# Performance work log

Hardware: AMD Instinct MI355X
Metric: run time of the kernel (lower is better)

## Reference

```python
import jax, jax.numpy as jnp
import numpy as np

LMAX = 3
D_IRREP = (LMAX + 1) ** 2  # 16
EPS = 1e-5


def _conv1d(x, w, pad):
    # x: [N, C_in, L], w: [C_out, C_in, K] -> [N, C_out, L]
    return jax.lax.conv_general_dilated(
        x, w, window_strides=(1,), padding=[(pad, pad)],
        dimension_numbers=("NCH", "OIH", "NCH"))


def setup_inputs() -> dict:
    key = jax.random.key(0)
    ks = jax.random.split(key, 8)
    B, Cin, Cout, N, K, RES = 128, 256, 256, 64, 5, 8
    return {
        "x": jax.random.normal(ks[0], (B, Cin * D_IRREP, N), jnp.float32),
        "weight": jax.random.normal(ks[1], (LMAX + 1, Cout, Cin, K), jnp.float32) / np.sqrt(Cin * K).astype(np.float32),
        "bias": jax.random.normal(ks[2], (1, 1, Cout), jnp.float32) * 0.02,
        "affine_weight": jnp.ones((LMAX + 1, Cout), jnp.float32),
        "gating_w": jax.random.normal(ks[3], (Cout, Cout), jnp.float32) / np.sqrt(Cout).astype(np.float32),
        "gating_b": jnp.zeros((Cout,), jnp.float32),
        "to_grid": jax.random.normal(ks[4], (RES, RES, D_IRREP), jnp.float32) * 0.3,
        "from_grid": jax.random.normal(ks[5], (RES, RES, D_IRREP), jnp.float32) * 0.3,
    }


def reference(x, weight, bias, affine_weight, gating_w, gating_b, to_grid, from_grid):
    B, CI, N = x.shape
    Cin = CI // D_IRREP
    Cout = weight.shape[1]
    pad = weight.shape[-1] // 2
    x = x.reshape(B, Cin, D_IRREP, N)

    # per-degree Conv1d over the time axis, irrep order folded into batch
    h_parts = []
    for l in range(LMAX + 1):
        lo, li = l * l, 2 * l + 1
        x_l = x[:, :, lo:lo + li, :]                                  # [B, Cin, li, N]
        x_l = x_l.transpose(0, 2, 1, 3).reshape(B * li, Cin, N)       # (b i) c n
        h_l = _conv1d(x_l, weight[l], pad)                            # [B*li, Cout, N]
        h_l = h_l.reshape(B, li, Cout, N).transpose(0, 3, 1, 2).reshape(B * N, li, Cout)  # (b n) i c
        if l == 0:
            h_l = h_l + bias
        h_parts.append(h_l)
    h = jnp.concatenate(h_parts, axis=1)                              # [B*N, 16, Cout]

    # rms_norm_sh: center l=0 over channels, degree-balanced RMS, per-degree affine
    degrees = np.repeat(np.arange(LMAX + 1), 2 * np.arange(LMAX + 1) + 1)  # [16]
    bal = jnp.asarray((1.0 / (2.0 * degrees + 1.0)) / (LMAX + 1), h.dtype)  # [16]
    mean0 = jnp.mean(h[:, :1, :], axis=2, keepdims=True)
    h = jnp.concatenate([h[:, :1, :] - mean0, h[:, 1:, :]], axis=1)
    var = jnp.einsum("zic,i->zc", h * h, bal)                         # [Z, C]
    inv = jax.lax.rsqrt(jnp.mean(var, axis=-1)[:, None, None] + EPS)  # [Z,1,1]
    h = h * inv * affine_weight[degrees][None]                        # [Z,16,C]

    # SeparableS2Activation: SiLU-gated scalars + S2 grid activation for l>0
    gate = jax.nn.silu(h[:, :1, :] @ gating_w.T + gating_b)           # [Z,1,C]
    grid = jax.nn.silu(jnp.einsum("bai,zic->zbac", to_grid, h))       # [Z,8,8,C]
    s2 = jnp.einsum("bai,zbac->zic", from_grid, grid)                 # [Z,16,C]
    h = jnp.concatenate([gate, s2[:, 1:, :]], axis=1)

    # (b n) i c -> b (c i) n
    out = h.reshape(B, N, D_IRREP, Cout).transpose(0, 3, 2, 1).reshape(B, Cout * D_IRREP, N)
    return out
```

## Files before the change

### kernel.cpp

```cpp
#include <hip/hip_runtime.h>
#include <hip/hip_bf16.h>

#define BB    128
#define CIN   256
#define COUT  256
#define NN    64
#define KW    5
#define DIRR  16
#define ZTOT  (BB*NN)
#define SX    264

typedef __attribute__((ext_vector_type(4))) float f32x4;
typedef __attribute__((ext_vector_type(8))) short s16x8;

__device__ inline ushort f2bf(float f) {
    __hip_bfloat16 h = __float2bfloat16(f);
    return *(const ushort*)&h;
}
__device__ inline float bf2f(ushort u) {
    union { unsigned int ui; float f; } cv; cv.ui = ((unsigned int)u) << 16;
    return cv.f;
}
__device__ inline float wave_sum(float v) {
    #pragma unroll
    for (int o = 32; o > 0; o >>= 1) v += __shfl_down(v, o, 64);
    return v;
}
__device__ inline float silu(float x) { return x / (1.f + __expf(-x)); }

__global__ __launch_bounds__(256) void pack_w_k(const float* __restrict__ w,
                                                ushort* __restrict__ wb)
{
    int idx = blockIdx.x * 256 + threadIdx.x;
    int cl = idx & 31;
    int c  = (idx >> 5) & 255;
    int ch = (idx >> 13) & 7;
    int k  = (idx >> 16) % 5;
    int l  = idx / 327680;
    int cin = ch * 32 + cl;
    wb[idx] = f2bf(w[(((size_t)(l * COUT + c) * CIN) + cin) * KW + k]);
}

__global__ __launch_bounds__(256) void pack2_k(const float* __restrict__ gw,
                                               const float* __restrict__ tg,
                                               const float* __restrict__ fg,
                                               ushort* __restrict__ gwb,
                                               ushort* __restrict__ tgb,
                                               ushort* __restrict__ fgTb)
{
    int idx = blockIdx.x * 256 + threadIdx.x;
    if (idx < 65536) {
        gwb[idx] = f2bf(gw[idx]);
    } else if (idx < 66560) {
        int j = idx - 65536;
        tgb[j] = f2bf(tg[j]);
    } else if (idx < 67584) {
        int j = idx - 66560;
        int p = j >> 4, i = j & 15;
        fgTb[i * 64 + p] = f2bf(fg[j]);
    }
}

__global__ __launch_bounds__(256, 4) void conv_mfma_k(const float* __restrict__ x,
                                                      const ushort* __restrict__ wb,
                                                      const float* __restrict__ bias,
                                                      ushort* __restrict__ hbuf)
{
    __shared__ __align__(16) ushort xs[68 * SX];

    const int tid  = threadIdx.x;
    const int lane = tid & 63;
    const int wid  = tid >> 6;
    const int blk  = blockIdx.x;
    const int b = blk >> 4, i = blk & 15;
    const int l = (i == 0) ? 0 : (i < 4) ? 1 : (i < 9) ? 2 : 3;

    {
        const float4* xb = (const float4*)(x + (((size_t)b * CIN) * DIRR + i) * NN);
        #pragma unroll
        for (int p = 0; p < 16; ++p) {
            int cin = (tid & 63) | ((p & 3) << 6);
            int nq  = ((tid >> 6) << 2) | (p >> 2);
            float4 v = xb[(size_t)cin * (DIRR * NN / 4) + nq];
            ushort* dst = xs + (size_t)(2 + nq * 4) * SX + cin;
            dst[0]      = f2bf(v.x);
            dst[SX]     = f2bf(v.y);
            dst[2 * SX] = f2bf(v.z);
            dst[3 * SX] = f2bf(v.w);
        }
        xs[ 0 * SX + tid] = 0; xs[ 1 * SX + tid] = 0;
        xs[66 * SX + tid] = 0; xs[67 * SX + tid] = 0;
    }
    __syncthreads();

    f32x4 acc[4][4];
    #pragma unroll
    for (int m = 0; m < 4; ++m)
        #pragma unroll
        for (int j = 0; j < 4; ++j) acc[m][j] = (f32x4){0.f, 0.f, 0.f, 0.f};

    const int kb = lane >> 4;
    const int lr = lane & 15;

    const ushort* wl = wb + (size_t)l * (40 * 8192);
    int boffB[4];
    #pragma unroll
    for (int j = 0; j < 4; ++j)
        boffB[j] = (wid * 64 + j * 16 + lr) * 32 + kb * 8;

    const ushort* arow = xs + (size_t)lr * SX + kb * 8;

    s16x8 bva[4], bvb[4];
    {
        const ushort* bt = wl;
        #pragma unroll
        for (int j = 0; j < 4; ++j) bva[j] = *(const s16x8*)(bt + boffB[j]);
    }

    #pragma unroll 1
    for (int t = 0; t < 40; t += 2) {
        {
            const ushort* bt = wl + ((size_t)(t + 1) << 13);
            #pragma unroll
            for (int j = 0; j < 4; ++j) bvb[j] = *(const s16x8*)(bt + boffB[j]);
        }
        {
            const ushort* ab = arow + (size_t)(t >> 3) * SX + (t & 7) * 32;
            s16x8 av[4];
            #pragma unroll
            for (int m = 0; m < 4; ++m)
                av[m] = *(const s16x8*)(ab + (size_t)m * 16 * SX);
            #pragma unroll
            for (int m = 0; m < 4; ++m)
                #pragma unroll
                for (int j = 0; j < 4; ++j)
                    acc[m][j] = __builtin_amdgcn_mfma_f32_16x16x32_bf16(av[m], bva[j], acc[m][j], 0, 0, 0);
        }
        if (t + 2 < 40) {
            const ushort* bt = wl + ((size_t)(t + 2) << 13);
            #pragma unroll
            for (int j = 0; j < 4; ++j) bva[j] = *(const s16x8*)(bt + boffB[j]);
        }
        {
            int t1 = t + 1;
            const ushort* ab = arow + (size_t)(t1 >> 3) * SX + (t1 & 7) * 32;
            s16x8 av[4];
            #pragma unroll
            for (int m = 0; m < 4; ++m)
                av[m] = *(const s16x8*)(ab + (size_t)m * 16 * SX);
            #pragma unroll
            for (int m = 0; m < 4; ++m)
                #pragma unroll
                for (int j = 0; j < 4; ++j)
                    acc[m][j] = __builtin_amdgcn_mfma_f32_16x16x32_bf16(av[m], bvb[j], acc[m][j], 0, 0, 0);
        }
    }

    const int row0 = (lane >> 4) * 4;
    #pragma unroll
    for (int j = 0; j < 4; ++j) {
        int c = wid * 64 + j * 16 + lr;
        float bvv = (i == 0) ? bias[c] : 0.f;
        #pragma unroll
        for (int m = 0; m < 4; ++m)
            #pragma unroll
            for (int r = 0; r < 4; ++r) {
                int n = m * 16 + row0 + r;
                size_t z = (size_t)b * NN + n;
                hbuf[(z * DIRR + i) * COUT + c] = f2bf(acc[m][j][r] + bvv);
            }
    }
}

__global__ __launch_bounds__(256) void norm_k(const ushort* __restrict__ hbuf,
                                              const float* __restrict__ afw,
                                              ushort* __restrict__ hn2,
                                              ushort* __restrict__ hn0)
{
    __shared__ float red[8];
    const int z0 = blockIdx.x * 2;
    const int c = threadIdx.x;
    const int lane = c & 63, w = c >> 6;

    float hv[2][16];
    #pragma unroll
    for (int zz = 0; zz < 2; ++zz)
        #pragma unroll
        for (int i = 0; i < 16; ++i)
            hv[zz][i] = bf2f(hbuf[((size_t)(z0 + zz) * DIRR + i) * COUT + c]);

    float s0 = wave_sum(hv[0][0]);
    float s1 = wave_sum(hv[1][0]);
    if (lane == 0) { red[w] = s0; red[4 + w] = s1; }
    __syncthreads();
    float m0 = (red[0] + red[1] + red[2] + red[3]) * (1.f / 256.f);
    float m1 = (red[4] + red[5] + red[6] + red[7]) * (1.f / 256.f);
    hv[0][0] -= m0;
    hv[1][0] -= m1;

    const float bal[4] = {0.25f, 1.f / 12.f, 1.f / 20.f, 1.f / 28.f};
    float var[2];
    #pragma unroll
    for (int zz = 0; zz < 2; ++zz) {
        float v = bal[0] * hv[zz][0] * hv[zz][0];
        #pragma unroll
        for (int i = 1; i < 16; ++i) {
            int li = (i < 4) ? 1 : (i < 9) ? 2 : 3;
            v += bal[li] * hv[zz][i] * hv[zz][i];
        }
        var[zz] = v;
    }
    float v0 = wave_sum(var[0]);
    float v1 = wave_sum(var[1]);
    __syncthreads();
    if (lane == 0) { red[w] = v0; red[4 + w] = v1; }
    __syncthreads();
    float inv[2];
    inv[0] = rsqrtf((red[0] + red[1] + red[2] + red[3]) * (1.f / 256.f) + 1e-5f);
    inv[1] = rsqrtf((red[4] + red[5] + red[6] + red[7]) * (1.f / 256.f) + 1e-5f);

    float a0 = afw[c], a1 = afw[COUT + c], a2 = afw[2 * COUT + c], a3 = afw[3 * COUT + c];
    #pragma unroll
    for (int zz = 0; zz < 2; ++zz) {
        s16x8 o0, o1;
        #pragma unroll
        for (int i = 0; i < 16; ++i) {
            float al = (i == 0) ? a0 : (i < 4) ? a1 : (i < 9) ? a2 : a3;
            ushort ub = f2bf(hv[zz][i] * inv[zz] * al);
            if (i < 8) o0[i] = (short)ub; else o1[i - 8] = (short)ub;
        }
        ushort* dst = hn2 + ((size_t)c * ZTOT + z0 + zz) * DIRR;
        *(s16x8*)dst = o0;
        *(s16x8*)(dst + 8) = o1;
        hn0[(size_t)(z0 + zz) * COUT + c] = (ushort)(unsigned short)o0[0];
    }
}

__global__ __launch_bounds__(256) void gate_k(const ushort* __restrict__ hn0,
                                              const ushort* __restrict__ gwb,
                                              const float* __restrict__ gb,
                                              float* __restrict__ out)
{
    const int b = blockIdx.x;
    const int tid = threadIdx.x;
    const int lane = tid & 63, w = tid >> 6;
    const int lr = lane & 15, kb = lane >> 4;

    f32x4 acc[4][4];
    #pragma unroll
    for (int m = 0; m < 4; ++m)
        #pragma unroll
        for (int n = 0; n < 4; ++n) acc[m][n] = (f32x4){0.f, 0.f, 0.f, 0.f};

    #pragma unroll 1
    for (int ks = 0; ks < 8; ++ks) {
        s16x8 av[4], bv[4];
        #pragma unroll
        for (int m = 0; m < 4; ++m)
            av[m] = *(const s16x8*)(hn0 + ((size_t)(b * 64 + m * 16 + lr) * 256 + ks * 32 + kb * 8));
        #pragma unroll
        for (int n = 0; n < 4; ++n)
            bv[n] = *(const s16x8*)(gwb + ((size_t)(w * 64 + n * 16 + lr) * 256 + ks * 32 + kb * 8));
        #pragma unroll
        for (int m = 0; m < 4; ++m)
            #pragma unroll
            for (int n = 0; n < 4; ++n)
                acc[m][n] = __builtin_amdgcn_mfma_f32_16x16x32_bf16(av[m], bv[n], acc[m][n], 0, 0, 0);
    }

    #pragma unroll
    for (int n = 0; n < 4; ++n) {
        int c = w * 64 + n * 16 + lr;
        float gbc = gb[c];
        #pragma unroll
        for (int m = 0; m < 4; ++m)
            #pragma unroll
            for (int r = 0; r < 4; ++r) {
                int nrow = m * 16 + kb * 4 + r;
                out[((size_t)b * COUT + c) * (DIRR * NN) + nrow] = silu(acc[m][n][r] + gbc);
            }
    }
}

__global__ __launch_bounds__(256) void grid_k(const ushort* __restrict__ hn2,
                                              const ushort* __restrict__ tgb,
                                              const ushort* __restrict__ fgTb,
                                              float* __restrict__ out)
{
    __shared__ __align__(16) char lds[36864 + 2048 + 2304];
    ushort* P_s  = (ushort*)lds;
    float*  S_s  = (float*)lds;
    ushort* tg_s = (ushort*)(lds + 36864);
    ushort* fgT_s= (ushort*)(lds + 36864 + 2048);

    const int bid = blockIdx.x;
    const int c  = bid & 255;
    const int zt = bid >> 8;
    const int z0 = zt * 256;
    const int tid = threadIdx.x;
    const int lane = tid & 63, w = tid >> 6;
    const int lr = lane & 15, kb = lane >> 4;

    #pragma unroll
    for (int q = 0; q < 4; ++q) {
        int idx = q * 256 + tid;
        tg_s[idx] = tgb[idx];
        int i = idx >> 6, p = idx & 63;
        fgT_s[i * 72 + p] = fgTb[idx];
    }
    __syncthreads();

    f32x4 acc[4][4];
    #pragma unroll
    for (int m = 0; m < 4; ++m)
        #pragma unroll
        for (int n = 0; n < 4; ++n) acc[m][n] = (f32x4){0.f, 0.f, 0.f, 0.f};

    s16x8 bv[4];
    #pragma unroll
    for (int n = 0; n < 4; ++n)
        bv[n] = (kb < 2) ? *(const s16x8*)(tg_s + (n * 16 + lr) * 16 + kb * 8)
                         : (s16x8){0,0,0,0,0,0,0,0};
    #pragma unroll
    for (int m = 0; m < 4; ++m) {
        int zl = w * 64 + m * 16 + lr;
        s16x8 av = (kb < 2) ? *(const s16x8*)(hn2 + ((size_t)c * ZTOT + z0 + zl) * DIRR + kb * 8)
                            : (s16x8){0,0,0,0,0,0,0,0};
        #pragma unroll
        for (int n = 0; n < 4; ++n)
            acc[m][n] = __builtin_amdgcn_mfma_f32_16x16x32_bf16(av, bv[n], acc[m][n], 0, 0, 0);
    }

    #pragma unroll
    for (int m = 0; m < 4; ++m)
        #pragma unroll
        for (int n = 0; n < 4; ++n)
            #pragma unroll
            for (int r = 0; r < 4; ++r) {
                int zl = w * 64 + m * 16 + kb * 4 + r;
                int p  = n * 16 + lr;
                P_s[zl * 72 + p] = f2bf(silu(acc[m][n][r]));
            }

    f32x4 acc2[4];
    #pragma unroll
    for (int m = 0; m < 4; ++m) acc2[m] = (f32x4){0.f, 0.f, 0.f, 0.f};
    #pragma unroll
    for (int ks = 0; ks < 2; ++ks) {
        s16x8 bv2 = *(const s16x8*)(fgT_s + lr * 72 + ks * 32 + kb * 8);
        #pragma unroll
        for (int m = 0; m < 4; ++m) {
            s16x8 av2 = *(const s16x8*)(P_s + (w * 64 + m * 16 + lr) * 72 + ks * 32 + kb * 8);
            acc2[m] = __builtin_amdgcn_mfma_f32_16x16x32_bf16(av2, bv2, acc2[m], 0, 0, 0);
        }
    }

    __syncthreads();

    #pragma unroll
    for (int m = 0; m < 4; ++m)
        #pragma unroll
        for (int r = 0; r < 4; ++r) {
            int zl = w * 64 + m * 16 + kb * 4 + r;
            S_s[zl * 17 + lr] = acc2[m][r];
        }
    __syncthreads();

    const int bb = tid >> 6, n = tid & 63;
    const int b0 = zt * 4;
    const float* srow = S_s + (bb * 64 + n) * 17;
    float* obase = out + ((size_t)(b0 + bb) * COUT + c) * (DIRR * NN) + n;
    #pragma unroll
    for (int i = 1; i < 16; ++i)
        obase[i * NN] = srow[i];
}

__global__ __launch_bounds__(256) void post_k(const ushort* __restrict__ hbuf,
                                              const float* __restrict__ afw,
                                              const float* __restrict__ gw,
                                              const float* __restrict__ gb,
                                              const float* __restrict__ tg,
                                              const float* __restrict__ fg,
                                              float* __restrict__ out)
{
    __shared__ float h0s[COUT];
    __shared__ float red[4];
    __shared__ float tgs[64 * 16];
    __shared__ float fgs[64 * 16];

    int z = blockIdx.x;
    int c = threadIdx.x;
    int b = z >> 6, n = z & 63;
    int lane = c & 63, wid = c >> 6;

    for (int idx = c; idx < 1024; idx += 256) { tgs[idx] = tg[idx]; fgs[idx] = fg[idx]; }

    float hv[16];
    #pragma unroll
    for (int i = 0; i < 16; ++i)
        hv[i] = bf2f(hbuf[((size_t)z * DIRR + i) * COUT + c]);

    float s0 = wave_sum(hv[0]);
    if (lane == 0) red[wid] = s0;
    __syncthreads();
    float mean0 = (red[0] + red[1] + red[2] + red[3]) * (1.f / 256.f);
    hv[0] -= mean0;

    const float bal[4] = {0.25f, 1.f / 12.f, 1.f / 20.f, 1.f / 28.f};
    float var = bal[0] * hv[0] * hv[0];
    #pragma unroll
    for (int i = 1; i < 16; ++i) {
        int li = (i < 4) ? 1 : (i < 9) ? 2 : 3;
        var += bal[li] * hv[i] * hv[i];
    }
    float s1 = wave_sum(var);
    __syncthreads();
    if (lane == 0) red[wid] = s1;
    __syncthreads();
    float inv = rsqrtf((red[0] + red[1] + red[2] + red[3]) * (1.f / 256.f) + 1e-5f);

    float a0 = afw[c], a1 = afw[COUT + c], a2 = afw[2 * COUT + c], a3 = afw[3 * COUT + c];
    #pragma unroll
    for (int i = 0; i < 16; ++i) {
        float al = (i == 0) ? a0 : (i < 4) ? a1 : (i < 9) ? a2 : a3;
        hv[i] *= inv * al;
    }
    h0s[c] = hv[0];
    __syncthreads();

    float g = gb[c];
    const float4* gwr = (const float4*)(gw + (size_t)c * COUT);
    #pragma unroll 4
    for (int j = 0; j < 64; ++j) {
        float4 wv = gwr[j];
        g += h0s[4 * j] * wv.x + h0s[4 * j + 1] * wv.y + h0s[4 * j + 2] * wv.z + h0s[4 * j + 3] * wv.w;
    }
    float gate = silu(g);

    float s2a[16];
    #pragma unroll
    for (int i = 0; i < 16; ++i) s2a[i] = 0.f;
    #pragma unroll 1
    for (int p = 0; p < 64; ++p) {
        float gv = 0.f;
        #pragma unroll
        for (int i = 0; i < 16; ++i) gv += tgs[p * 16 + i] * hv[i];
        gv = silu(gv);
        #pragma unroll
        for (int i = 0; i < 16; ++i) s2a[i] += fgs[p * 16 + i] * gv;
    }

    float* ob = out + (size_t)b * COUT * DIRR * NN + (size_t)c * DIRR * NN + n;
    ob[0] = gate;
    #pragma unroll
    for (int i = 1; i < 16; ++i) ob[i * NN] = s2a[i];
}

extern "C" void kernel_launch(void* const* d_in, const int* in_sizes, int n_in,
                              void* d_out, int out_size, void* d_ws, size_t ws_size,
                              hipStream_t stream)
{
    const float* x    = (const float*)d_in[0];
    const float* w    = (const float*)d_in[1];
    const float* bias = (const float*)d_in[2];
    const float* afw  = (const float*)d_in[3];
    const float* gw   = (const float*)d_in[4];
    const float* gb   = (const float*)d_in[5];
    const float* tg   = (const float*)d_in[6];
    const float* fg   = (const float*)d_in[7];
    float* out = (float*)d_out;

    const size_t off_hbuf = 0;
    const size_t off_wb   = 67108864;
    const size_t off_hn2  = 69730304;
    const size_t off_hn0  = off_hn2 + 67108864;
    const size_t off_gwb  = off_hn0 + 4194304;
    const size_t off_tgb  = off_gwb + 131072;
    const size_t off_fgT  = off_tgb + 2048;
    const size_t need     = off_fgT + 2048;

    ushort* hbuf = (ushort*)((char*)d_ws + off_hbuf);
    ushort* wb   = (ushort*)((char*)d_ws + off_wb);

    pack_w_k   <<<5120, 256, 0, stream>>>(w, wb);
    conv_mfma_k<<<BB * DIRR, 256, 0, stream>>>(x, wb, bias, hbuf);

    if (ws_size >= need) {
        ushort* hn2  = (ushort*)((char*)d_ws + off_hn2);
        ushort* hn0  = (ushort*)((char*)d_ws + off_hn0);
        ushort* gwb  = (ushort*)((char*)d_ws + off_gwb);
        ushort* tgb  = (ushort*)((char*)d_ws + off_tgb);
        ushort* fgTb = (ushort*)((char*)d_ws + off_fgT);

        pack2_k<<<264, 256, 0, stream>>>(gw, tg, fg, gwb, tgb, fgTb);
        norm_k <<<ZTOT / 2, 256, 0, stream>>>(hbuf, afw, hn2, hn0);
        gate_k <<<BB, 256, 0, stream>>>(hn0, gwb, gb, out);
        grid_k <<<256 * (ZTOT / 256), 256, 0, stream>>>(hn2, tgb, fgTb, out);
    } else {
        post_k<<<ZTOT, 256, 0, stream>>>(hbuf, afw, gw, gb, tg, fg, out);
    }
}
```

Baseline: 256.3 us.

## Process two batches per conv block to reuse weight fragments across batches

Each conv block now handles two batch elements, so every loaded weight fragment feeds MFMAs for both batches. This halves the global weight traffic per output. Input channels are staged through shared memory in two halves to keep LDS size bounded, and input loads become nontemporal. The grid is halved and launch bounds drop to 2 blocks per CU, because the doubled accumulators raise register pressure and cut occupancy.

```diff
diff --git a/kernel.cpp b/kernel.cpp
--- a/kernel.cpp
+++ b/kernel.cpp
@@ -8,7 +8,7 @@
 #define KW    5
 #define DIRR  16
 #define ZTOT  (BB*NN)
-#define SX    264
+#define SX2   136
 
 typedef __attribute__((ext_vector_type(4))) float f32x4;
 typedef __attribute__((ext_vector_type(8))) short s16x8;
@@ -61,43 +61,20 @@
     }
 }
 
-__global__ __launch_bounds__(256, 4) void conv_mfma_k(const float* __restrict__ x,
+__global__ __launch_bounds__(256, 2) void conv_mfma_k(const float* __restrict__ x,
                                                       const ushort* __restrict__ wb,
                                                       const float* __restrict__ bias,
                                                       ushort* __restrict__ hbuf)
 {
-    __shared__ __align__(16) ushort xs[68 * SX];
+    __shared__ __align__(16) ushort xs[2 * 68 * SX2];
 
     const int tid  = threadIdx.x;
     const int lane = tid & 63;
     const int wid  = tid >> 6;
     const int blk  = blockIdx.x;
-    const int b = blk >> 4, i = blk & 15;
+    const int bp = blk >> 4, i = blk & 15;
+    const int b0 = bp * 2;
     const int l = (i == 0) ? 0 : (i < 4) ? 1 : (i < 9) ? 2 : 3;
-
-    {
-        const float4* xb = (const float4*)(x + (((size_t)b * CIN) * DIRR + i) * NN);
-        #pragma unroll
-        for (int p = 0; p < 16; ++p) {
-            int cin = (tid & 63) | ((p & 3) << 6);
-            int nq  = ((tid >> 6) << 2) | (p >> 2);
-            float4 v = xb[(size_t)cin * (DIRR * NN / 4) + nq];
-            ushort* dst = xs + (size_t)(2 + nq * 4) * SX + cin;
-            dst[0]      = f2bf(v.x);
-            dst[SX]     = f2bf(v.y);
-            dst[2 * SX] = f2bf(v.z);
-            dst[3 * SX] = f2bf(v.w);
-        }
-        xs[ 0 * SX + tid] = 0; xs[ 1 * SX + tid] = 0;
-        xs[66 * SX + tid] = 0; xs[67 * SX + tid] = 0;
-    }
-    __syncthreads();
-
-    f32x4 acc[4][4];
-    #pragma unroll
-    for (int m = 0; m < 4; ++m)
-        #pragma unroll
-        for (int j = 0; j < 4; ++j) acc[m][j] = (f32x4){0.f, 0.f, 0.f, 0.f};
 
     const int kb = lane >> 4;
     const int lr = lane & 15;
@@ -108,67 +85,110 @@
     for (int j = 0; j < 4; ++j)
         boffB[j] = (wid * 64 + j * 16 + lr) * 32 + kb * 8;
 
-    const ushort* arow = xs + (size_t)lr * SX + kb * 8;
+    f32x4 acc[2][4][4];
+    #pragma unroll
+    for (int bb = 0; bb < 2; ++bb)
+        #pragma unroll
+        for (int m = 0; m < 4; ++m)
+            #pragma unroll
+            for (int j = 0; j < 4; ++j) acc[bb][m][j] = (f32x4){0.f, 0.f, 0.f, 0.f};
 
     s16x8 bva[4], bvb[4];
-    {
-        const ushort* bt = wl;
-        #pragma unroll
-        for (int j = 0; j < 4; ++j) bva[j] = *(const s16x8*)(bt + boffB[j]);
-    }
-
-    #pragma unroll 1
-    for (int t = 0; t < 40; t += 2) {
-        {
-            const ushort* bt = wl + ((size_t)(t + 1) << 13);
-            #pragma unroll
-            for (int j = 0; j < 4; ++j) bvb[j] = *(const s16x8*)(bt + boffB[j]);
-        }
-        {
-            const ushort* ab = arow + (size_t)(t >> 3) * SX + (t & 7) * 32;
+
+    auto mstep = [&](const s16x8* bv, int s, int che) {
+        const int col = che * 32 + kb * 8;
+        #pragma unroll
+        for (int bb = 0; bb < 2; ++bb) {
+            const ushort* ab = xs + ((size_t)bb * 68 + lr + s) * SX2 + col;
             s16x8 av[4];
             #pragma unroll
             for (int m = 0; m < 4; ++m)
-                av[m] = *(const s16x8*)(ab + (size_t)m * 16 * SX);
+                av[m] = *(const s16x8*)(ab + (size_t)m * 16 * SX2);
             #pragma unroll
             for (int m = 0; m < 4; ++m)
                 #pragma unroll
                 for (int j = 0; j < 4; ++j)
-                    acc[m][j] = __builtin_amdgcn_mfma_f32_16x16x32_bf16(av[m], bva[j], acc[m][j], 0, 0, 0);
-        }
-        if (t + 2 < 40) {
-            const ushort* bt = wl + ((size_t)(t + 2) << 13);
+                    acc[bb][m][j] = __builtin_amdgcn_mfma_f32_16x16x32_bf16(av[m], bv[j], acc[bb][m][j], 0, 0, 0);
+        }
+    };
+
+    #pragma unroll 1
+    for (int hh = 0; hh < 2; ++hh) {
+        __syncthreads();
+        #pragma unroll
+        for (int bb = 0; bb < 2; ++bb) {
+            const f32x4* xb = (const f32x4*)(x + (((size_t)(b0 + bb) * CIN) * DIRR + i) * NN);
+            #pragma unroll
+            for (int p = 0; p < 8; ++p) {
+                int cl  = (tid & 63) | ((p & 1) << 6);
+                int nq  = ((tid >> 6) << 2) | (p >> 1);
+                int cin = hh * 128 + cl;
+                f32x4 v = __builtin_nontemporal_load(xb + (size_t)cin * (DIRR * NN / 4) + nq);
+                ushort* dst = xs + ((size_t)bb * 68 + 2 + nq * 4) * SX2 + cl;
+                dst[0]       = f2bf(v.x);
+                dst[SX2]     = f2bf(v.y);
+                dst[2 * SX2] = f2bf(v.z);
+                dst[3 * SX2] = f2bf(v.w);
+            }
+        }
+        #pragma unroll
+        for (int q = 0; q < 4; ++q) {
+            int idx = q * 256 + tid;
+            int cl = idx & 127;
+            int rr = (idx >> 7) & 3;
+            int bb = idx >> 9;
+            int row = (rr < 2) ? rr : (64 + rr);
+            xs[((size_t)bb * 68 + row) * SX2 + cl] = 0;
+        }
+        __syncthreads();
+
+        const ushort* wlh = wl + (size_t)hh * 4 * 8192;
+        {
+            const ushort* bt = wlh;
             #pragma unroll
             for (int j = 0; j < 4; ++j) bva[j] = *(const s16x8*)(bt + boffB[j]);
         }
-        {
-            int t1 = t + 1;
-            const ushort* ab = arow + (size_t)(t1 >> 3) * SX + (t1 & 7) * 32;
-            s16x8 av[4];
-            #pragma unroll
-            for (int m = 0; m < 4; ++m)
-                av[m] = *(const s16x8*)(ab + (size_t)m * 16 * SX);
+        #pragma unroll 1
+        for (int s = 0; s < 5; ++s) {
+            const ushort* bs0 = wlh + ((size_t)s * 8 << 13);
+            {
+                #pragma unroll
+                for (int j = 0; j < 4; ++j) bvb[j] = *(const s16x8*)(bs0 + (1 << 13) + boffB[j]);
+                mstep(bva, s, 0);
+                #pragma unroll
+                for (int j = 0; j < 4; ++j) bva[j] = *(const s16x8*)(bs0 + (2 << 13) + boffB[j]);
+                mstep(bvb, s, 1);
+            }
+            {
+                #pragma unroll
+                for (int j = 0; j < 4; ++j) bvb[j] = *(const s16x8*)(bs0 + (3 << 13) + boffB[j]);
+                mstep(bva, s, 2);
+                if (s < 4) {
+                    const ushort* bn = bs0 + ((size_t)8 << 13);
+                    #pragma unroll
+                    for (int j = 0; j < 4; ++j) bva[j] = *(const s16x8*)(bn + boffB[j]);
+                }
+                mstep(bvb, s, 3);
+            }
+        }
+    }
+
+    const int row0 = (lane >> 4) * 4;
+    #pragma unroll
+    for (int bb = 0; bb < 2; ++bb) {
+        #pragma unroll
+        for (int j = 0; j < 4; ++j) {
+            int c = wid * 64 + j * 16 + lr;
+            float bvv = (i == 0) ? bias[c] : 0.f;
             #pragma unroll
             for (int m = 0; m < 4; ++m)
                 #pragma unroll
-                for (int j = 0; j < 4; ++j)
-                    acc[m][j] = __builtin_amdgcn_mfma_f32_16x16x32_bf16(av[m], bvb[j], acc[m][j], 0, 0, 0);
-        }
-    }
-
-    const int row0 = (lane >> 4) * 4;
-    #pragma unroll
-    for (int j = 0; j < 4; ++j) {
-        int c = wid * 64 + j * 16 + lr;
-        float bvv = (i == 0) ? bias[c] : 0.f;
-        #pragma unroll
-        for (int m = 0; m < 4; ++m)
-            #pragma unroll
-            for (int r = 0; r < 4; ++r) {
-                int n = m * 16 + row0 + r;
-                size_t z = (size_t)b * NN + n;
-                hbuf[(z * DIRR + i) * COUT + c] = f2bf(acc[m][j][r] + bvv);
-            }
+                for (int r = 0; r < 4; ++r) {
+                    int n = m * 16 + row0 + r;
+                    size_t z = (size_t)(b0 + bb) * NN + n;
+                    hbuf[(z * DIRR + i) * COUT + c] = f2bf(acc[bb][m][j][r] + bvv);
+                }
+        }
     }
 }
 
@@ -483,7 +503,7 @@
     ushort* wb   = (ushort*)((char*)d_ws + off_wb);
 
     pack_w_k   <<<5120, 256, 0, stream>>>(w, wb);
-    conv_mfma_k<<<BB * DIRR, 256, 0, stream>>>(x, wb, bias, hbuf);
+    conv_mfma_k<<<(BB / 2) * DIRR, 256, 0, stream>>>(x, wb, bias, hbuf);
 
     if (ws_size >= need) {
         ushort* hn2  = (ushort*)((char*)d_ws + off_hn2);
```

Result: slower. 307.6 us (+20.0%).
